# Performance work log

Hardware: AMD Instinct MI355X
Metric: run time of the kernel (lower is better)

The kernel has to match this reference:

```python
import jax, jax.numpy as jnp
import numpy as np

N = 50000        # nodes
E = 800000       # edges (before self-loops)
IN = 512         # in_channels
HEADS = 8        # 'head' arg: heads and per-head out dim of conv1
C1 = 8           # per-head channels of conv1 (== head)
OUT = 128        # out_channels of conv2
NEG_SLOPE = 0.2  # PyG GATConv leaky-relu slope


def _glorot(key, shape, fan_in):
    return jax.random.normal(key, shape, jnp.float32) * (1.0 / np.sqrt(fan_in))


def setup_inputs() -> dict:
    key = jax.random.key(0)
    ks = jax.random.split(key, 10)
    x = jax.random.normal(ks[0], (N, IN), jnp.float32)
    edge_index = jax.random.randint(ks[1], (2, E), 0, N, dtype=jnp.int32)
    # conv1: GATConv(IN, C1, heads=HEADS, concat=True)
    W1 = _glorot(ks[2], (IN, HEADS * C1), IN)
    att_src1 = _glorot(ks[3], (HEADS, C1), C1)
    att_dst1 = _glorot(ks[4], (HEADS, C1), C1)
    bias1 = jnp.zeros((HEADS * C1,), jnp.float32)
    # conv2: GATConv(HEADS*C1, OUT, heads=1, concat=False)
    W2 = _glorot(ks[5], (HEADS * C1, OUT), HEADS * C1)
    att_src2 = _glorot(ks[6], (1, OUT), OUT)
    att_dst2 = _glorot(ks[7], (1, OUT), OUT)
    bias2 = jnp.zeros((OUT,), jnp.float32)
    return {"x": x, "edge_index": edge_index,
            "W1": W1, "att_src1": att_src1, "att_dst1": att_dst1, "bias1": bias1,
            "W2": W2, "att_src2": att_src2, "att_dst2": att_dst2, "bias2": bias2}


def gat_conv(x, src, dst, W, a_src, a_dst, bias, heads, concat):
    """PyG GATConv (eval mode, dropout off). src/dst already include self-loops."""
    n = x.shape[0]
    h = (x @ W).reshape(n, heads, -1)                 # [N, H, C]
    s = (h * a_src[None]).sum(-1)                     # [N, H] alpha_src per node
    d = (h * a_dst[None]).sum(-1)                     # [N, H] alpha_dst per node
    alpha = jax.nn.leaky_relu(s[src] + d[dst], NEG_SLOPE)  # [E, H]
    # segment softmax over incoming edges of each destination node
    amax = jax.ops.segment_max(alpha, dst, num_segments=n)  # [N, H]
    amax = jnp.where(jnp.isfinite(amax), amax, 0.0)
    ea = jnp.exp(alpha - amax[dst])                   # [E, H]
    denom = jax.ops.segment_sum(ea, dst, num_segments=n)
    w = ea / (denom[dst] + 1e-16)                     # [E, H]
    msg = h[src] * w[..., None]                       # [E, H, C]
    out = jax.ops.segment_sum(msg, dst, num_segments=n)  # [N, H, C]
    out = out.reshape(n, -1) if concat else out.mean(axis=1)
    return out + bias


def reference(x, edge_index, W1, att_src1, att_dst1, bias1,
              W2, att_src2, att_dst2, bias2):
    n = x.shape[0]
    loop = jnp.arange(n, dtype=edge_index.dtype)      # PyG adds self-loops
    src = jnp.concatenate([edge_index[0], loop])
    dst = jnp.concatenate([edge_index[1], loop])
    h = jax.nn.elu(gat_conv(x, src, dst, W1, att_src1, att_dst1, bias1,
                            heads=HEADS, concat=True))
    out = jax.nn.elu(gat_conv(h, src, dst, W2, att_src2, att_dst2, bias2,
                              heads=1, concat=False))
    return out
```

## Files before the change

### kernel.cpp

```cpp
#include <hip/hip_runtime.h>

#define NEG_SLOPE 0.2f

typedef __attribute__((ext_vector_type(8))) short bf16x8;
typedef __attribute__((ext_vector_type(4))) float f32x4;

__device__ __forceinline__ float leaky(float v) {
    return v > 0.0f ? v : NEG_SLOPE * v;
}
__device__ __forceinline__ float elu(float v) {
    return v > 0.0f ? v : (__expf(v) - 1.0f);
}
__device__ __forceinline__ short f2b(float f) {
    return (short)((__float_as_uint(f) + 0x8000u) >> 16);
}
__device__ __forceinline__ float bf2f(unsigned short v) {
    return __uint_as_float(((unsigned)v) << 16);
}

__global__ void prep_k(const float* __restrict__ W1, const float* __restrict__ W2,
                       unsigned short* __restrict__ w1s, unsigned short* __restrict__ w2s,
                       int* __restrict__ deg, int N) {
    int i = blockIdx.x * 256 + threadIdx.x;
    if (i <= N) deg[i] = 0;
    if (i < 512 * 64) {
        int k = i >> 6, n = i & 63;
        int kt = k >> 5, kk = k & 31;
        int nt = n >> 4, nn = n & 15;
        int lane = (kk >> 3) * 16 + nn, j = kk & 7;
        w1s[(((size_t)(kt * 4 + nt)) * 64 + lane) * 8 + j] = (unsigned short)f2b(W1[i]);
    } else if (i < 512 * 64 + 64 * 128) {
        int i2 = i - 512 * 64;
        int k = i2 >> 7, n = i2 & 127;
        int kt = k >> 5, kk = k & 31;
        int nt = n >> 4, nn = n & 15;
        int lane = (kk >> 3) * 16 + nn, j = kk & 7;
        w2s[(((size_t)(kt * 8 + nt)) * 64 + lane) * 8 + j] = (unsigned short)f2b(W2[i2]);
    }
}

__global__ __launch_bounds__(256) void g1deg_k(const float* __restrict__ X,
                                               const unsigned short* __restrict__ Ws,
                                               const float* __restrict__ Asrc,
                                               const float* __restrict__ Adst,
                                               unsigned short* __restrict__ Hb,
                                               float* __restrict__ S,
                                               float* __restrict__ D,
                                               const int* __restrict__ dst,
                                               int* __restrict__ deg,
                                               int N, int E, int gblk) {
    if ((int)blockIdx.x >= gblk) {
        int wtid = ((int)blockIdx.x - gblk) * 256 + threadIdx.x;
        int base = wtid * 8;
        if (base + 8 <= E) {
            int4 a = *(const int4*)(dst + base);
            int4 b = *(const int4*)(dst + base + 4);
            atomicAdd(&deg[a.x], 1); atomicAdd(&deg[a.y], 1);
            atomicAdd(&deg[a.z], 1); atomicAdd(&deg[a.w], 1);
            atomicAdd(&deg[b.x], 1); atomicAdd(&deg[b.y], 1);
            atomicAdd(&deg[b.z], 1); atomicAdd(&deg[b.w], 1);
        } else {
            for (int e = base; e < E; ++e) atomicAdd(&deg[dst[e]], 1);
        }
        return;
    }
    const int lane = threadIdx.x & 63;
    const int wave = threadIdx.x >> 6;
    const int m0 = blockIdx.x * 64 + wave * 16;
    const int q = lane >> 4, lc = lane & 15;
    const int arow = m0 + lc;
    const float* xrow = X + (size_t)min(arow, N - 1) * 512 + q * 8;
    const bf16x8* bW = (const bf16x8*)Ws;

    f32x4 acc[4] = {{0.f,0.f,0.f,0.f},{0.f,0.f,0.f,0.f},{0.f,0.f,0.f,0.f},{0.f,0.f,0.f,0.f}};

    for (int kt = 0; kt < 16; ++kt) {
        float4 a0 = *(const float4*)(xrow + kt * 32);
        float4 a1 = *(const float4*)(xrow + kt * 32 + 4);
        bf16x8 af;
        af[0] = f2b(a0.x); af[1] = f2b(a0.y); af[2] = f2b(a0.z); af[3] = f2b(a0.w);
        af[4] = f2b(a1.x); af[5] = f2b(a1.y); af[6] = f2b(a1.z); af[7] = f2b(a1.w);
#pragma unroll
        for (int nt = 0; nt < 4; ++nt) {
            bf16x8 bf = bW[(size_t)(kt * 4 + nt) * 64 + lane];
            acc[nt] = __builtin_amdgcn_mfma_f32_16x16x32_bf16(af, bf, acc[nt], 0, 0, 0);
        }
    }

    float asc[4], adc[4];
#pragma unroll
    for (int nt = 0; nt < 4; ++nt) { asc[nt] = Asrc[nt * 16 + lc]; adc[nt] = Adst[nt * 16 + lc]; }

#pragma unroll
    for (int r = 0; r < 4; ++r) {
        int row = m0 + q * 4 + r;
        bool ok = row < N;
        if (ok) {
#pragma unroll
            for (int nt = 0; nt < 4; ++nt)
                Hb[(size_t)row * 64 + nt * 16 + lc] = (unsigned short)f2b(acc[nt][r]);
        }
        float ps[4], pd[4];
#pragma unroll
        for (int nt = 0; nt < 4; ++nt) { ps[nt] = acc[nt][r] * asc[nt]; pd[nt] = acc[nt][r] * adc[nt]; }
#pragma unroll
        for (int off = 1; off < 8; off <<= 1) {
#pragma unroll
            for (int nt = 0; nt < 4; ++nt) {
                ps[nt] += __shfl_xor(ps[nt], off);
                pd[nt] += __shfl_xor(pd[nt], off);
            }
        }
        if (ok && !(lc & 7)) {
            int hb = lc >> 3;
#pragma unroll
            for (int nt = 0; nt < 4; ++nt) {
                S[(size_t)row * 8 + nt * 2 + hb] = ps[nt];
                D[(size_t)row * 8 + nt * 2 + hb] = pd[nt];
            }
        }
    }
}

__global__ __launch_bounds__(256) void scan_k(const int* __restrict__ deg_in,
                                              int* __restrict__ ticket,
                                              int* __restrict__ beg,
                                              int* __restrict__ wp,
                                              int* __restrict__ srcs, int N) {
    __shared__ int sm[256];
    __shared__ int chunkBase;
    const int t = threadIdx.x;
    int idx = blockIdx.x * 1024 + t * 4;
    int v[4];
#pragma unroll
    for (int i = 0; i < 4; ++i) v[i] = (idx + i < N) ? deg_in[idx + i] + 1 : 0;
    int sum = v[0] + v[1] + v[2] + v[3];
    sm[t] = sum;
    __syncthreads();
    for (int off = 1; off < 256; off <<= 1) {
        int xv = (t >= off) ? sm[t - off] : 0;
        __syncthreads();
        sm[t] += xv;
        __syncthreads();
    }
    if (t == 255) chunkBase = atomicAdd(ticket, sm[255]);
    __syncthreads();
    int run = chunkBase + sm[t] - sum;
#pragma unroll
    for (int i = 0; i < 4; ++i) {
        if (idx + i < N) {
            beg[idx + i] = run;
            srcs[run] = idx + i;
            wp[idx + i] = run + 1;
            run += v[i];
        }
    }
}

__global__ void scatter_k(const int* __restrict__ ei, int E,
                          int* __restrict__ wp, int* __restrict__ srcs) {
    int base = (blockIdx.x * blockDim.x + threadIdx.x) * 4;
    if (base + 4 <= E) {
        int4 s = *(const int4*)(ei + base);
        int4 d = *(const int4*)(ei + E + base);
        int p0 = atomicAdd(&wp[d.x], 1);
        int p1 = atomicAdd(&wp[d.y], 1);
        int p2 = atomicAdd(&wp[d.z], 1);
        int p3 = atomicAdd(&wp[d.w], 1);
        srcs[p0] = s.x; srcs[p1] = s.y; srcs[p2] = s.z; srcs[p3] = s.w;
    } else {
        for (int e = base; e < E; ++e) {
            int p = atomicAdd(&wp[ei[E + e]], 1);
            srcs[p] = ei[e];
        }
    }
}

__global__ __launch_bounds__(256) void agg1g2_k(const int* __restrict__ beg,
                                                const int* __restrict__ deg,
                                                const int* __restrict__ srcs,
                                                const float* __restrict__ S1,
                                                const float* __restrict__ D1,
                                                const unsigned short* __restrict__ H1b,
                                                const float* __restrict__ b1,
                                                const unsigned short* __restrict__ W2s,
                                                const float* __restrict__ as2,
                                                const float* __restrict__ ad2,
                                                unsigned short* __restrict__ H2b,
                                                float* __restrict__ S2,
                                                float* __restrict__ D2, int N) {
    __shared__ unsigned short sh[16][64];
    __shared__ float shp[4][16], shq[4][16];

    const int tid  = threadIdx.x;
    const int lane = tid & 63;
    const int wave = tid >> 6;
    const int m0 = blockIdx.x * 16;

    const int h = lane & 7;
    const int el = lane >> 3;
#pragma unroll
    for (int rep = 0; rep < 4; ++rep) {
        const int nl = wave * 4 + rep;
        const int wid = m0 + nl;
        if (wid < N) {
            const int b0 = beg[wid];
            const int e0 = b0 + deg[wid] + 1;
            const float dvh = D1[(size_t)wid * 8 + h];

            float m = -1e30f;
            for (int i = b0 + el; i < e0; i += 8)
                m = fmaxf(m, leaky(S1[(size_t)srcs[i] * 8 + h] + dvh));
#pragma unroll
            for (int off = 8; off < 64; off <<= 1)
                m = fmaxf(m, __shfl_xor(m, off));

            float acc = 0.0f, den = 0.0f;
            for (int base = b0; base < e0; base += 8) {
                int i = base + el;
                int src_l = 0; float w_l = 0.0f;
                if (i < e0) {
                    src_l = srcs[i];
                    w_l = __expf(leaky(S1[(size_t)src_l * 8 + h] + dvh) - m);
                }
                den += w_l;
#pragma unroll
                for (int j = 0; j < 8; ++j) {
                    float w = __shfl(w_l, j * 8 + (lane >> 3));
                    int src = __builtin_amdgcn_readfirstlane(__shfl(src_l, j * 8));
                    acc += w * bf2f(H1b[(size_t)src * 64 + lane]);
                }
            }
#pragma unroll
            for (int off = 8; off < 64; off <<= 1)
                den += __shfl_xor(den, off);
            float rden = 1.0f / (__shfl(den, lane >> 3) + 1e-16f);
            sh[nl][lane] = (unsigned short)f2b(elu(acc * rden + b1[lane]));
        } else {
            sh[nl][lane] = 0;
        }
    }
    __syncthreads();

    const int q = lane >> 4, lc = lane & 15;
    const bf16x8* bW = (const bf16x8*)W2s;
    const int nt0 = wave * 2;

    f32x4 acc2[2] = {{0.f,0.f,0.f,0.f},{0.f,0.f,0.f,0.f}};
#pragma unroll
    for (int kt = 0; kt < 2; ++kt) {
        bf16x8 af = *(const bf16x8*)(&sh[lc][q * 8 + kt * 32]);
#pragma unroll
        for (int u = 0; u < 2; ++u) {
            bf16x8 bf = bW[(size_t)(kt * 8 + nt0 + u) * 64 + lane];
            acc2[u] = __builtin_amdgcn_mfma_f32_16x16x32_bf16(af, bf, acc2[u], 0, 0, 0);
        }
    }
    float asc[2], adc[2];
#pragma unroll
    for (int u = 0; u < 2; ++u) {
        asc[u] = as2[(nt0 + u) * 16 + lc];
        adc[u] = ad2[(nt0 + u) * 16 + lc];
    }
#pragma unroll
    for (int r = 0; r < 4; ++r) {
        int rl = q * 4 + r;
        int row = m0 + rl;
        if (row < N) {
#pragma unroll
            for (int u = 0; u < 2; ++u)
                H2b[(size_t)row * 128 + (nt0 + u) * 16 + lc] = (unsigned short)f2b(acc2[u][r]);
        }
        float ps = acc2[0][r] * asc[0] + acc2[1][r] * asc[1];
        float pd = acc2[0][r] * adc[0] + acc2[1][r] * adc[1];
#pragma unroll
        for (int off = 1; off < 16; off <<= 1) {
            ps += __shfl_xor(ps, off);
            pd += __shfl_xor(pd, off);
        }
        if (lc == 0) { shp[wave][rl] = ps; shq[wave][rl] = pd; }
    }
    __syncthreads();
    if (tid < 16) {
        int row = m0 + tid;
        if (row < N) {
            float s = shp[0][tid] + shp[1][tid] + shp[2][tid] + shp[3][tid];
            float d = shq[0][tid] + shq[1][tid] + shq[2][tid] + shq[3][tid];
            S2[row] = s;
            D2[row] = d;
        }
    }
}

__global__ __launch_bounds__(256) void agg2_csr_k(const int* __restrict__ beg,
                                                  const int* __restrict__ deg,
                                                  const int* __restrict__ srcs,
                                                  const float* __restrict__ S,
                                                  const float* __restrict__ D,
                                                  const unsigned short* __restrict__ Hb,
                                                  const float* __restrict__ bias,
                                                  float* __restrict__ out, int N) {
    const int wid = (blockIdx.x * 256 + threadIdx.x) >> 6;
    const int lane = threadIdx.x & 63;
    if (wid >= N) return;
    const int b0 = beg[wid];
    const int e0 = b0 + deg[wid] + 1;
    const float dv = D[wid];
    const int c0 = lane * 2;

    float m = -1e30f;
    for (int i = b0 + lane; i < e0; i += 64)
        m = fmaxf(m, leaky(S[srcs[i]] + dv));
#pragma unroll
    for (int off = 1; off < 64; off <<= 1)
        m = fmaxf(m, __shfl_xor(m, off));

    float acc0 = 0.0f, acc1 = 0.0f, den = 0.0f;
    for (int base = b0; base < e0; base += 64) {
        int i = base + lane;
        int src_l = 0; float w_l = 0.0f;
        if (i < e0) {
            src_l = srcs[i];
            w_l = __expf(leaky(S[src_l] + dv) - m);
        }
        den += w_l;
        const int cnt = min(64, e0 - base);
        for (int j0 = 0; j0 < cnt; j0 += 8) {
#pragma unroll
            for (int u = 0; u < 8; ++u) {
                int j = j0 + u;
                float w = __shfl(w_l, j);
                int src = __builtin_amdgcn_readfirstlane(__shfl(src_l, j));
                unsigned pv = *(const unsigned*)(Hb + (size_t)src * 128 + c0);
                acc0 += w * __uint_as_float(pv << 16);
                acc1 += w * __uint_as_float(pv & 0xffff0000u);
            }
        }
    }
#pragma unroll
    for (int off = 1; off < 64; off <<= 1)
        den += __shfl_xor(den, off);
    const float rden = 1.0f / (den + 1e-16f);
    float2 o;
    o.x = elu(acc0 * rden + bias[c0]);
    o.y = elu(acc1 * rden + bias[c0 + 1]);
    *(float2*)(out + (size_t)wid * 128 + c0) = o;
}

extern "C" void kernel_launch(void* const* d_in, const int* in_sizes, int n_in,
                              void* d_out, int out_size, void* d_ws, size_t ws_size,
                              hipStream_t stream) {
    const float* x   = (const float*)d_in[0];
    const int*   ei  = (const int*)d_in[1];
    const float* W1  = (const float*)d_in[2];
    const float* as1 = (const float*)d_in[3];
    const float* ad1 = (const float*)d_in[4];
    const float* b1  = (const float*)d_in[5];
    const float* W2  = (const float*)d_in[6];
    const float* as2 = (const float*)d_in[7];
    const float* ad2 = (const float*)d_in[8];
    const float* b2  = (const float*)d_in[9];

    const int N = in_sizes[0] / 512;
    const int E = in_sizes[1] / 2;

    unsigned short* w1s  = (unsigned short*)d_ws;
    unsigned short* w2s  = w1s + 512 * 64;
    unsigned short* h1b  = w2s + 64 * 128;
    unsigned short* h2b  = h1b + (size_t)N * 64;
    float*          s1   = (float*)(h2b + (size_t)N * 128);
    float*          d1   = s1 + (size_t)N * 8;
    float*          s2   = d1 + (size_t)N * 8;
    float*          d2   = s2 + N;
    int*            beg  = (int*)(d2 + N);
    int*            deg  = beg + N;
    int*            wp   = deg + (N + 1);
    int*            srcs = wp + N;

    const int B = 256;
    const int gblk = (N + 63) / 64;
    const int degb = (E / 8 + B - 1) / B;
    const int nb   = (N + 1023) / 1024;
    int prep_n = 512 * 64 + 64 * 128;
    if (N + 1 > prep_n) prep_n = N + 1;

    prep_k<<<(prep_n + B - 1) / B, B, 0, stream>>>(W1, W2, w1s, w2s, deg, N);
    g1deg_k<<<gblk + degb, B, 0, stream>>>(x, w1s, as1, ad1, h1b, s1, d1,
                                           ei + E, deg, N, E, gblk);
    scan_k<<<nb, B, 0, stream>>>(deg, deg + N, beg, wp, srcs, N);
    scatter_k<<<(E + B * 4 - 1) / (B * 4), B, 0, stream>>>(ei, E, wp, srcs);
    agg1g2_k<<<(N + 15) / 16, B, 0, stream>>>(beg, deg, srcs, s1, d1, h1b, b1,
                                              w2s, as2, ad2, h2b, s2, d2, N);
    agg2_csr_k<<<(N + 3) / 4, B, 0, stream>>>(beg, deg, srcs, s2, d2, h2b, b2,
                                              (float*)d_out, N);
}
```

Before: 354.9 us.

## Co-schedule the conv1 GEMM with the edge scatter instead of the degree count

The degree-count atomics move into their own small kernel ahead of the scan. The layer-1 MFMA projection is now fused with the CSR scatter pass rather than with the degree histogram, so the memory-heavy GEMM overlaps with the heavier atomic scatter. The GEMM loop is also restructured to load eight float4s of X per group of four k-tiles, giving more loads in flight. The kernel count stays the same, but the longer fused kernel now sits after the scan, and register pressure rises from the batched loads.

```diff
diff --git a/kernel.cpp b/kernel.cpp
--- a/kernel.cpp
+++ b/kernel.cpp
@@ -39,86 +39,17 @@
     }
 }
 
-__global__ __launch_bounds__(256) void g1deg_k(const float* __restrict__ X,
-                                               const unsigned short* __restrict__ Ws,
-                                               const float* __restrict__ Asrc,
-                                               const float* __restrict__ Adst,
-                                               unsigned short* __restrict__ Hb,
-                                               float* __restrict__ S,
-                                               float* __restrict__ D,
-                                               const int* __restrict__ dst,
-                                               int* __restrict__ deg,
-                                               int N, int E, int gblk) {
-    if ((int)blockIdx.x >= gblk) {
-        int wtid = ((int)blockIdx.x - gblk) * 256 + threadIdx.x;
-        int base = wtid * 8;
-        if (base + 8 <= E) {
-            int4 a = *(const int4*)(dst + base);
-            int4 b = *(const int4*)(dst + base + 4);
-            atomicAdd(&deg[a.x], 1); atomicAdd(&deg[a.y], 1);
-            atomicAdd(&deg[a.z], 1); atomicAdd(&deg[a.w], 1);
-            atomicAdd(&deg[b.x], 1); atomicAdd(&deg[b.y], 1);
-            atomicAdd(&deg[b.z], 1); atomicAdd(&deg[b.w], 1);
-        } else {
-            for (int e = base; e < E; ++e) atomicAdd(&deg[dst[e]], 1);
-        }
-        return;
-    }
-    const int lane = threadIdx.x & 63;
-    const int wave = threadIdx.x >> 6;
-    const int m0 = blockIdx.x * 64 + wave * 16;
-    const int q = lane >> 4, lc = lane & 15;
-    const int arow = m0 + lc;
-    const float* xrow = X + (size_t)min(arow, N - 1) * 512 + q * 8;
-    const bf16x8* bW = (const bf16x8*)Ws;
-
-    f32x4 acc[4] = {{0.f,0.f,0.f,0.f},{0.f,0.f,0.f,0.f},{0.f,0.f,0.f,0.f},{0.f,0.f,0.f,0.f}};
-
-    for (int kt = 0; kt < 16; ++kt) {
-        float4 a0 = *(const float4*)(xrow + kt * 32);
-        float4 a1 = *(const float4*)(xrow + kt * 32 + 4);
-        bf16x8 af;
-        af[0] = f2b(a0.x); af[1] = f2b(a0.y); af[2] = f2b(a0.z); af[3] = f2b(a0.w);
-        af[4] = f2b(a1.x); af[5] = f2b(a1.y); af[6] = f2b(a1.z); af[7] = f2b(a1.w);
-#pragma unroll
-        for (int nt = 0; nt < 4; ++nt) {
-            bf16x8 bf = bW[(size_t)(kt * 4 + nt) * 64 + lane];
-            acc[nt] = __builtin_amdgcn_mfma_f32_16x16x32_bf16(af, bf, acc[nt], 0, 0, 0);
-        }
-    }
-
-    float asc[4], adc[4];
-#pragma unroll
-    for (int nt = 0; nt < 4; ++nt) { asc[nt] = Asrc[nt * 16 + lc]; adc[nt] = Adst[nt * 16 + lc]; }
-
-#pragma unroll
-    for (int r = 0; r < 4; ++r) {
-        int row = m0 + q * 4 + r;
-        bool ok = row < N;
-        if (ok) {
-#pragma unroll
-            for (int nt = 0; nt < 4; ++nt)
-                Hb[(size_t)row * 64 + nt * 16 + lc] = (unsigned short)f2b(acc[nt][r]);
-        }
-        float ps[4], pd[4];
-#pragma unroll
-        for (int nt = 0; nt < 4; ++nt) { ps[nt] = acc[nt][r] * asc[nt]; pd[nt] = acc[nt][r] * adc[nt]; }
-#pragma unroll
-        for (int off = 1; off < 8; off <<= 1) {
-#pragma unroll
-            for (int nt = 0; nt < 4; ++nt) {
-                ps[nt] += __shfl_xor(ps[nt], off);
-                pd[nt] += __shfl_xor(pd[nt], off);
-            }
-        }
-        if (ok && !(lc & 7)) {
-            int hb = lc >> 3;
-#pragma unroll
-            for (int nt = 0; nt < 4; ++nt) {
-                S[(size_t)row * 8 + nt * 2 + hb] = ps[nt];
-                D[(size_t)row * 8 + nt * 2 + hb] = pd[nt];
-            }
-        }
+__global__ void deg_k(const int* __restrict__ dst, int E, int* __restrict__ deg) {
+    int base = (blockIdx.x * blockDim.x + threadIdx.x) * 8;
+    if (base + 8 <= E) {
+        int4 a = *(const int4*)(dst + base);
+        int4 b = *(const int4*)(dst + base + 4);
+        atomicAdd(&deg[a.x], 1); atomicAdd(&deg[a.y], 1);
+        atomicAdd(&deg[a.z], 1); atomicAdd(&deg[a.w], 1);
+        atomicAdd(&deg[b.x], 1); atomicAdd(&deg[b.y], 1);
+        atomicAdd(&deg[b.z], 1); atomicAdd(&deg[b.w], 1);
+    } else {
+        for (int e = base; e < E; ++e) atomicAdd(&deg[dst[e]], 1);
     }
 }
 
@@ -157,21 +88,97 @@
     }
 }
 
-__global__ void scatter_k(const int* __restrict__ ei, int E,
-                          int* __restrict__ wp, int* __restrict__ srcs) {
-    int base = (blockIdx.x * blockDim.x + threadIdx.x) * 4;
-    if (base + 4 <= E) {
-        int4 s = *(const int4*)(ei + base);
-        int4 d = *(const int4*)(ei + E + base);
-        int p0 = atomicAdd(&wp[d.x], 1);
-        int p1 = atomicAdd(&wp[d.y], 1);
-        int p2 = atomicAdd(&wp[d.z], 1);
-        int p3 = atomicAdd(&wp[d.w], 1);
-        srcs[p0] = s.x; srcs[p1] = s.y; srcs[p2] = s.z; srcs[p3] = s.w;
-    } else {
-        for (int e = base; e < E; ++e) {
-            int p = atomicAdd(&wp[ei[E + e]], 1);
-            srcs[p] = ei[e];
+__global__ __launch_bounds__(256) void g1scat_k(const float* __restrict__ X,
+                                                const unsigned short* __restrict__ Ws,
+                                                const float* __restrict__ Asrc,
+                                                const float* __restrict__ Adst,
+                                                unsigned short* __restrict__ Hb,
+                                                float* __restrict__ S,
+                                                float* __restrict__ D,
+                                                const int* __restrict__ ei,
+                                                int* __restrict__ wp,
+                                                int* __restrict__ srcs,
+                                                int N, int E, int gblk) {
+    if ((int)blockIdx.x >= gblk) {
+        int wtid = ((int)blockIdx.x - gblk) * 256 + threadIdx.x;
+        int base = wtid * 4;
+        if (base + 4 <= E) {
+            int4 s = *(const int4*)(ei + base);
+            int4 d = *(const int4*)(ei + E + base);
+            int p0 = atomicAdd(&wp[d.x], 1);
+            int p1 = atomicAdd(&wp[d.y], 1);
+            int p2 = atomicAdd(&wp[d.z], 1);
+            int p3 = atomicAdd(&wp[d.w], 1);
+            srcs[p0] = s.x; srcs[p1] = s.y; srcs[p2] = s.z; srcs[p3] = s.w;
+        } else {
+            for (int e = base; e < E; ++e) {
+                int p = atomicAdd(&wp[ei[E + e]], 1);
+                srcs[p] = ei[e];
+            }
+        }
+        return;
+    }
+    const int lane = threadIdx.x & 63;
+    const int wave = threadIdx.x >> 6;
+    const int m0 = blockIdx.x * 64 + wave * 16;
+    const int q = lane >> 4, lc = lane & 15;
+    const int arow = m0 + lc;
+    const float* xrow = X + (size_t)min(arow, N - 1) * 512 + q * 8;
+    const bf16x8* bW = (const bf16x8*)Ws;
+
+    f32x4 acc[4] = {{0.f,0.f,0.f,0.f},{0.f,0.f,0.f,0.f},{0.f,0.f,0.f,0.f},{0.f,0.f,0.f,0.f}};
+
+    for (int g = 0; g < 4; ++g) {
+        float4 a[8];
+#pragma unroll
+        for (int u = 0; u < 8; ++u)
+            a[u] = *(const float4*)(xrow + g * 128 + (u >> 1) * 32 + (u & 1) * 4);
+#pragma unroll
+        for (int u2 = 0; u2 < 4; ++u2) {
+            const int kt = g * 4 + u2;
+            float4 a0 = a[u2 * 2], a1 = a[u2 * 2 + 1];
+            bf16x8 af;
+            af[0] = f2b(a0.x); af[1] = f2b(a0.y); af[2] = f2b(a0.z); af[3] = f2b(a0.w);
+            af[4] = f2b(a1.x); af[5] = f2b(a1.y); af[6] = f2b(a1.z); af[7] = f2b(a1.w);
+#pragma unroll
+            for (int nt = 0; nt < 4; ++nt) {
+                bf16x8 bf = bW[(size_t)(kt * 4 + nt) * 64 + lane];
+                acc[nt] = __builtin_amdgcn_mfma_f32_16x16x32_bf16(af, bf, acc[nt], 0, 0, 0);
+            }
+        }
+    }
+
+    float asc[4], adc[4];
+#pragma unroll
+    for (int nt = 0; nt < 4; ++nt) { asc[nt] = Asrc[nt * 16 + lc]; adc[nt] = Adst[nt * 16 + lc]; }
+
+#pragma unroll
+    for (int r = 0; r < 4; ++r) {
+        int row = m0 + q * 4 + r;
+        bool ok = row < N;
+        if (ok) {
+#pragma unroll
+            for (int nt = 0; nt < 4; ++nt)
+                Hb[(size_t)row * 64 + nt * 16 + lc] = (unsigned short)f2b(acc[nt][r]);
+        }
+        float ps[4], pd[4];
+#pragma unroll
+        for (int nt = 0; nt < 4; ++nt) { ps[nt] = acc[nt][r] * asc[nt]; pd[nt] = acc[nt][r] * adc[nt]; }
+#pragma unroll
+        for (int off = 1; off < 8; off <<= 1) {
+#pragma unroll
+            for (int nt = 0; nt < 4; ++nt) {
+                ps[nt] += __shfl_xor(ps[nt], off);
+                pd[nt] += __shfl_xor(pd[nt], off);
+            }
+        }
+        if (ok && !(lc & 7)) {
+            int hb = lc >> 3;
+#pragma unroll
+            for (int nt = 0; nt < 4; ++nt) {
+                S[(size_t)row * 8 + nt * 2 + hb] = ps[nt];
+                D[(size_t)row * 8 + nt * 2 + hb] = pd[nt];
+            }
         }
     }
 }
@@ -378,17 +385,17 @@
     int*            srcs = wp + N;
 
     const int B = 256;
-    const int gblk = (N + 63) / 64;
-    const int degb = (E / 8 + B - 1) / B;
-    const int nb   = (N + 1023) / 1024;
+    const int gblk  = (N + 63) / 64;
+    const int scatb = (E + B * 4 - 1) / (B * 4);
+    const int nb    = (N + 1023) / 1024;
     int prep_n = 512 * 64 + 64 * 128;
     if (N + 1 > prep_n) prep_n = N + 1;
 
     prep_k<<<(prep_n + B - 1) / B, B, 0, stream>>>(W1, W2, w1s, w2s, deg, N);
-    g1deg_k<<<gblk + degb, B, 0, stream>>>(x, w1s, as1, ad1, h1b, s1, d1,
-                                           ei + E, deg, N, E, gblk);
+    deg_k<<<(E + B * 8 - 1) / (B * 8), B, 0, stream>>>(ei + E, E, deg);
     scan_k<<<nb, B, 0, stream>>>(deg, deg + N, beg, wp, srcs, N);
-    scatter_k<<<(E + B * 4 - 1) / (B * 4), B, 0, stream>>>(ei, E, wp, srcs);
+    g1scat_k<<<gblk + scatb, B, 0, stream>>>(x, w1s, as1, ad1, h1b, s1, d1,
+                                             ei, wp, srcs, N, E, gblk);
     agg1g2_k<<<(N + 15) / 16, B, 0, stream>>>(beg, deg, srcs, s1, d1, h1b, b1,
                                               w2s, as2, ad2, h2b, s2, d2, N);
     agg2_csr_k<<<(N + 3) / 4, B, 0, stream>>>(beg, deg, srcs, s2, d2, h2b, b2,
```

New measurement: 358.2 us. About the same (+0.9%).
